# Optimization experiments

Measured on AMD Instinct MI355X. Metric: run time of the kernel, lower is better.

The kernel has to match this reference:

```python
import jax, jax.numpy as jnp
import numpy as np

B, N, D = 64, 512, 768


def setup_inputs() -> dict:
    key = jax.random.key(0)
    k = jax.random.split(key, 7)
    x = jax.random.normal(k[0], (B, N, D), dtype=jnp.float32)
    adj = jax.random.normal(k[1], (B, N, N), dtype=jnp.float32)
    # additive BERT-style mask: 0 for valid tokens, -10000 for padding
    lengths = jax.random.randint(k[2], (B,), N // 2, N + 1)
    valid = jnp.arange(N)[None, :] < lengths[:, None]          # [B, N]
    mask = jnp.where(valid, 0.0, -10000.0).astype(jnp.float32).reshape(B, 1, 1, N)
    roots_label = (jax.random.uniform(k[3], (B, N)) < 0.1).astype(jnp.float32)
    root_mask = valid.astype(jnp.int32)
    w_root = jax.random.normal(k[4], (D,), dtype=jnp.float32) / np.sqrt(D)
    b_root = jnp.zeros((), dtype=jnp.float32)
    return {"x": x, "adj": adj, "mask": mask, "roots_label": roots_label,
            "root_mask": root_mask, "w_root": w_root, "b_root": b_root}


def _matrix_tree_multi(scores, root):
    # scores: [B,N,N], root: [B,N]
    A = jnp.exp(scores)
    R = jnp.exp(root)
    L = jnp.sum(A, axis=1)                     # column sums (torch dim=1)
    LL = jnp.zeros_like(A).at[:, jnp.arange(A.shape[1]), jnp.arange(A.shape[1])].set(L + R) - A
    # equivalent to diag(L) - A + diag(R); keep diag of -A zeroed by set:
    LL = (jnp.apply_along_axis(jnp.diag, 1, np.zeros((1,))) if False else LL)  # no-op
    LL = jax.vmap(jnp.diag)(L + R) - A + jax.vmap(jnp.diag)(jnp.diagonal(A, axis1=1, axis2=2))
    # Recompute cleanly to match torch exactly: LL = diag(L) - A + diag(R)
    LL = jax.vmap(jnp.diag)(L) - A + jax.vmap(jnp.diag)(R)
    LL_inv = jnp.linalg.inv(LL)                # [B,N,N]
    LL_inv_diag = jnp.diagonal(LL_inv, axis1=1, axis2=2)   # [B,N]
    d0 = R * LL_inv_diag                       # root marginals [B,N]
    tmp1 = A * LL_inv_diag[:, None, :]         # A[i,j] * diag[j]
    tmp2 = A * jnp.swapaxes(LL_inv, 1, 2)      # A[i,j] * LL_inv[j,i]
    d = tmp1 - tmp2                            # edge marginals [B,N,N]
    return d, d0


def reference(x, adj, mask, roots_label, root_mask, w_root, b_root):
    root = jnp.einsum("bnd,d->bn", x, w_root) + b_root          # [B,N]
    m = mask[:, 0] / -10000.0                                    # [B,1,N], 0 valid / 1 pad
    root = jnp.maximum(root - m[:, 0, :] * 50.0, -40.0)
    scores = adj - m * 50.0 - jnp.swapaxes(m, 1, 2) * 50.0
    scores = jnp.maximum(scores, -40.0)
    d, d0 = _matrix_tree_multi(scores, root)
    # BCE root loss
    active = root_mask.reshape(-1) == 1
    labels = jnp.where(active, roots_label.reshape(-1), 0.0).astype(jnp.float32)
    logits = jnp.clip(d0.reshape(-1), 1e-5, 1.0 - 1e-5).astype(jnp.float32)
    bce = -(labels * jnp.log(logits) + (1.0 - labels) * jnp.log(1.0 - logits))
    loss_root = jnp.mean(bce * root_mask.reshape(-1).astype(jnp.float32))
    # attention = d^T with padded key columns zeroed
    attn = jnp.swapaxes(d, 1, 2)
    pad = jnp.broadcast_to(m.astype(bool), scores.shape)         # [B,N,N]
    attn = jnp.where(pad, 0.0, attn)
    context = jnp.matmul(attn, x)                                # [B,N,D]
    return context, d, loss_root
```

## Files before the change

kernel.cpp:

```cpp
#include <hip/hip_runtime.h>
#include <cstdint>
#include <cstddef>

#define BB 64
#define NN 512
#define DD 768
#define KB 64
#define NSTEP (NN/KB)

typedef __bf16 bf16x8 __attribute__((ext_vector_type(8)));
typedef float f32x4 __attribute__((ext_vector_type(4)));
typedef unsigned short us8 __attribute__((ext_vector_type(8)));
typedef double f64x4 __attribute__((ext_vector_type(4)));
typedef double f64x2 __attribute__((ext_vector_type(2)));

__device__ __forceinline__ float aval(float adjv, float mi, float mj) {
    return expf(fmaxf(adjv - 50.f * (mi + mj), -40.f));
}

__device__ __forceinline__ unsigned short f2bf(float v) {
    union { float f; unsigned int u; } c; c.f = v;
    return (unsigned short)((c.u + 0x7fffu + ((c.u >> 16) & 1u)) >> 16);
}
__device__ __forceinline__ float bf2f(unsigned short h) {
    union { unsigned int u; float f; } c; c.u = ((unsigned int)h) << 16;
    return c.f;
}

__device__ __forceinline__ void gl_lds16(const void* g, void* l) {
    __builtin_amdgcn_global_load_lds((const __attribute__((address_space(1))) unsigned int*)g,
                                     (__attribute__((address_space(3))) unsigned int*)l, 16, 0, 0);
}

__global__ void k_root(const float* __restrict__ x, const float* __restrict__ mask,
                       const float* __restrict__ w, const float* __restrict__ br,
                       float* __restrict__ R) {
    int wave = threadIdx.x >> 6, lane = threadIdx.x & 63;
    int row = blockIdx.x * 4 + wave;
    const float* xr = x + (size_t)row * DD;
    float s = 0.f;
#pragma unroll
    for (int k = 0; k < DD / 64; ++k) s += xr[k * 64 + lane] * w[k * 64 + lane];
    for (int off = 32; off; off >>= 1) s += __shfl_down(s, off, 64);
    if (lane == 0) {
        float m = mask[row] * -1e-4f;
        float rv = fmaxf(s + br[0] - 50.f * m, -40.f);
        R[row] = expf(rv);
    }
}

__global__ void k_colsum(const float* __restrict__ adj, const float* __restrict__ mask,
                         double* __restrict__ Lp) {
    int b = blockIdx.x, chunk = blockIdx.y;
    int j = threadIdx.x;
    float mj = mask[b * NN + j] * -1e-4f;
    const float* ab = adj + (size_t)b * NN * NN;
    double acc = 0.0;
    int i0 = chunk * 128;
    for (int i = i0; i < i0 + 128; ++i) {
        float mi = mask[b * NN + i] * -1e-4f;
        acc += (double)aval(ab[(size_t)i * NN + j], mi, mj);
    }
    Lp[((size_t)b * 4 + chunk) * NN + j] = acc;
}

template <typename T>
__global__ void k_build(const float* __restrict__ adj, const float* __restrict__ mask,
                        const float* __restrict__ R, const double* __restrict__ Lp,
                        T* __restrict__ M) {
    int b = blockIdx.x >> 9;
    int r = blockIdx.x & 511;
    int c = threadIdx.x;
    float mr = mask[b * NN + r] * -1e-4f;
    float mc = mask[b * NN + c] * -1e-4f;
    size_t idx = ((size_t)b * NN + r) * NN + c;
    float a = aval(adj[idx], mr, mc);
    T v;
    if (r == c) {
        const double* lp = Lp + (size_t)b * 4 * NN;
        double L = lp[c] + lp[NN + c] + lp[2 * NN + c] + lp[3 * NN + c];
        v = (T)(L - (double)a + (double)R[b * NN + c]);
    } else {
        v = (T)(-a);
    }
    M[idx] = v;
}

template <typename T>
__global__ void k_savecol(const T* __restrict__ M, T* __restrict__ Cb, int k0) {
    int t = threadIdx.x;
    int c = t & 63, rr = t >> 6;
    int row = blockIdx.x * 4 + rr;
    int b = row >> 9, i = row & 511;
    Cb[(size_t)row * KB + c] = M[((size_t)b * NN + i) * NN + k0 + c];
}

template <typename T>
__global__ void k_invblk(const T* __restrict__ M, T* __restrict__ Bb, int k0) {
    __shared__ double pr[KB];
    __shared__ double fv[KB];
    __shared__ double pvt;
    int b = blockIdx.x;
    int r = threadIdx.x & 63, q = threadIdx.x >> 6;
    double a[16];
    const T* Mb = M + ((size_t)b * NN + k0) * NN + k0;
#pragma unroll
    for (int c = 0; c < 16; ++c) a[c] = (double)Mb[(size_t)r * NN + q * 16 + c];
    for (int k = 0; k < KB; ++k) {
        int kq = k >> 4, kc = k & 15;
        if (r == k && q == kq) pvt = a[kc];
        __syncthreads();
        double ip = 1.0 / pvt;
        if (r == k) {
#pragma unroll
            for (int c = 0; c < 16; ++c) a[c] *= ip;
            if (q == kq) a[kc] = ip;
#pragma unroll
            for (int c = 0; c < 16; ++c) pr[q * 16 + c] = a[c];
        }
        if (r != k && q == kq) fv[r] = a[kc];
        __syncthreads();
        if (r != k) {
            double f = fv[r];
#pragma unroll
            for (int c = 0; c < 16; ++c) a[c] -= f * pr[q * 16 + c];
            if (q == kq) a[kc] = -f * ip;
        }
        __syncthreads();
    }
    T* Bo = Bb + (size_t)b * KB * KB;
#pragma unroll
    for (int c = 0; c < 16; ++c) Bo[r * KB + q * 16 + c] = (T)a[c];
}

__global__ __launch_bounds__(256) void k_piv_mfma(double* __restrict__ M,
                                                  const double* __restrict__ Bb, int step) {
    __shared__ double Ms[64][66];
    int o = blockIdx.x;
    int g = (o & 7) * 64 + (o >> 3);
    int b = g >> 3, jt = g & 7;
    int t = threadIdx.x, w = t >> 6, l = t & 63;
    double* Mb = M + (size_t)b * NN * NN;
    double* Pr = Mb + (size_t)(step * 64) * NN;
    const double* Bi = Bb + (size_t)b * KB * KB;
    if (jt == step) {
        for (int i = 0; i < 16; ++i) {
            int c = i * 256 + t;
            int row = c >> 6, col = c & 63;
            Pr[(size_t)row * NN + step * 64 + col] = Bi[row * 64 + col];
        }
        return;
    }
    const double* Mg = Pr + jt * 64;
    for (int i = 0; i < 8; ++i) {
        int c = i * 256 + t;
        int row = c >> 5, ch = c & 31;
        f64x2 v = *(const f64x2*)(Mg + (size_t)row * NN + ch * 2);
        Ms[row][ch * 2] = v[0]; Ms[row][ch * 2 + 1] = v[1];
    }
    __syncthreads();
    int lr = l & 15, lg = l >> 4;
    double a[16];
#pragma unroll
    for (int kk = 0; kk < 16; ++kk) a[kk] = Bi[(w * 16 + lr) * 64 + kk * 4 + lg];
    double* Og = Pr + (size_t)(w * 16) * NN + jt * 64;
#pragma unroll
    for (int cf = 0; cf < 4; ++cf) {
        f64x4 acc = {0., 0., 0., 0.};
#pragma unroll
        for (int kk = 0; kk < 16; ++kk)
            acc = __builtin_amdgcn_mfma_f64_16x16x4f64(a[kk], Ms[kk * 4 + lg][cf * 16 + lr], acc, 0, 0, 0);
#pragma unroll
        for (int r = 0; r < 4; ++r) Og[(size_t)(lg + 4 * r) * NN + cf * 16 + lr] = acc[r];
    }
}

__global__ __launch_bounds__(256) void k_upd2(double* __restrict__ M,
                                              const double* __restrict__ Bb, int step) {
    __shared__ double Ts[64][66];
    int o = blockIdx.x;
    int g = (o & 7) * 112 + (o >> 3);
    int b = g / 14;
    int x = g % 14;
    int it = x >> 1, half = x & 1;
    if (it >= step) ++it;
    int t = threadIdx.x, w = t >> 6, l = t & 63;
    double* Mb = M + (size_t)b * NN * NN;
    {
        const double* Cg = Mb + (size_t)(it * 64) * NN + step * 64;
        for (int i = 0; i < 8; ++i) {
            int c = i * 256 + t;
            int row = c >> 5, ch = c & 31;
            f64x2 v = *(const f64x2*)(Cg + (size_t)row * NN + ch * 2);
            Ts[row][ch * 2] = -v[0]; Ts[row][ch * 2 + 1] = -v[1];
        }
    }
    __syncthreads();
    int lr = l & 15, lg = l >> 4;
    double a[16];
#pragma unroll
    for (int kk = 0; kk < 16; ++kk) a[kk] = Ts[w * 16 + lr][kk * 4 + lg];
    __syncthreads();
    int nj = half ? 3 : 4;
    for (int jj = 0; jj < nj; ++jj) {
        int jtidx = half ? 4 + jj : jj;
        int jt = (jtidx < step) ? jtidx : jtidx + 1;
        const double* Rg = Mb + (size_t)(step * 64) * NN + jt * 64;
        for (int i = 0; i < 8; ++i) {
            int c = i * 256 + t;
            int row = c >> 5, ch = c & 31;
            f64x2 v = *(const f64x2*)(Rg + (size_t)row * NN + ch * 2);
            Ts[row][ch * 2] = v[0]; Ts[row][ch * 2 + 1] = v[1];
        }
        __syncthreads();
        double* Og = Mb + (size_t)(it * 64 + w * 16) * NN + jt * 64;
#pragma unroll
        for (int cf = 0; cf < 4; ++cf) {
            int c0 = cf * 16 + lr;
            f64x4 acc;
#pragma unroll
            for (int r = 0; r < 4; ++r) acc[r] = Og[(size_t)(lg + 4 * r) * NN + c0];
#pragma unroll
            for (int kk = 0; kk < 16; ++kk)
                acc = __builtin_amdgcn_mfma_f64_16x16x4f64(a[kk], Ts[kk * 4 + lg][c0], acc, 0, 0, 0);
#pragma unroll
            for (int r = 0; r < 4; ++r) Og[(size_t)(lg + 4 * r) * NN + c0] = acc[r];
        }
        __syncthreads();
    }
    if (half) {
        const double* Bi = Bb + (size_t)b * KB * KB;
        for (int i = 0; i < 8; ++i) {
            int c = i * 256 + t;
            int row = c >> 5, ch = c & 31;
            f64x2 v = *(const f64x2*)(Bi + row * 64 + ch * 2);
            Ts[row][ch * 2] = v[0]; Ts[row][ch * 2 + 1] = v[1];
        }
        __syncthreads();
        double* Og = Mb + (size_t)(it * 64 + w * 16) * NN + step * 64;
#pragma unroll
        for (int cf = 0; cf < 4; ++cf) {
            int c0 = cf * 16 + lr;
            f64x4 acc = {0., 0., 0., 0.};
#pragma unroll
            for (int kk = 0; kk < 16; ++kk)
                acc = __builtin_amdgcn_mfma_f64_16x16x4f64(a[kk], Ts[kk * 4 + lg][c0], acc, 0, 0, 0);
#pragma unroll
            for (int r = 0; r < 4; ++r) Og[(size_t)(lg + 4 * r) * NN + c0] = acc[r];
        }
    }
}

template <typename T>
__global__ void k_pivrows(T* __restrict__ M, const T* __restrict__ Bb, int k0) {
    __shared__ double Bi[KB][KB];
    __shared__ double Mt[KB][KB + 1];
    int b = blockIdx.x, jt = blockIdx.y * 64;
    const T* Bo = Bb + (size_t)b * KB * KB;
    T* Mb = M + ((size_t)b * NN + k0) * NN;
    int t = threadIdx.x;
    for (int e = t; e < KB * KB; e += 256) {
        int rr = e >> 6, cc = e & 63;
        Bi[rr][cc] = (double)Bo[e];
        Mt[rr][cc] = (double)Mb[(size_t)rr * NN + jt + cc];
    }
    __syncthreads();
    if (blockIdx.y == (unsigned)(k0 >> 6)) {
        for (int e = t; e < KB * KB; e += 256) {
            int rr = e >> 6, cc = e & 63;
            Mb[(size_t)rr * NN + jt + cc] = (T)Bi[rr][cc];
        }
        return;
    }
    int tx = t & 15, ty = t >> 4;
    double acc[4][4] = {};
    for (int k = 0; k < KB; ++k) {
        double av[4], bv[4];
#pragma unroll
        for (int u = 0; u < 4; ++u) { av[u] = Bi[ty * 4 + u][k]; bv[u] = Mt[k][tx * 4 + u]; }
#pragma unroll
        for (int u = 0; u < 4; ++u)
#pragma unroll
            for (int v = 0; v < 4; ++v) acc[u][v] += av[u] * bv[v];
    }
#pragma unroll
    for (int u = 0; u < 4; ++u)
#pragma unroll
        for (int v = 0; v < 4; ++v)
            Mb[(size_t)(ty * 4 + u) * NN + jt + tx * 4 + v] = (T)acc[u][v];
}

template <typename T>
__global__ void k_update(T* __restrict__ M, const T* __restrict__ Cb, int k0) {
    int step = k0 >> 6;
    int it = blockIdx.y;
    if (it == step) return;
    int b = blockIdx.x, jt = blockIdx.z;
    __shared__ double Ct[KB][KB + 1];
    __shared__ double Rt[KB][KB + 1];
    int t = threadIdx.x;
    const T* Cbb = Cb + ((size_t)b * NN + it * 64) * KB;
    const T* Rb  = M + ((size_t)b * NN + k0) * NN + jt * 64;
    for (int e = t; e < KB * KB; e += 256) {
        int rr = e >> 6, cc = e & 63;
        Ct[rr][cc] = (double)Cbb[(size_t)rr * KB + cc];
        Rt[rr][cc] = (double)Rb[(size_t)rr * NN + cc];
    }
    __syncthreads();
    int tx = t & 15, ty = t >> 4;
    double acc[4][4] = {};
    for (int k = 0; k < KB; ++k) {
        double av[4], bv[4];
#pragma unroll
        for (int u = 0; u < 4; ++u) { av[u] = Ct[ty * 4 + u][k]; bv[u] = Rt[k][tx * 4 + u]; }
#pragma unroll
        for (int u = 0; u < 4; ++u)
#pragma unroll
            for (int v = 0; v < 4; ++v) acc[u][v] += av[u] * bv[v];
    }
    T* Mo = M + ((size_t)b * NN + it * 64) * NN + jt * 64;
    bool blockcol = (jt == step);
#pragma unroll
    for (int u = 0; u < 4; ++u) {
        int row = ty * 4 + u;
#pragma unroll
        for (int v = 0; v < 4; ++v) {
            int col = tx * 4 + v;
            double val = (double)Mo[(size_t)row * NN + col] - acc[u][v];
            if (blockcol) val -= Ct[row][col];
            Mo[(size_t)row * NN + col] = (T)val;
        }
    }
}

template <typename T>
__global__ void k_dgloss(const T* __restrict__ M, const float* __restrict__ R,
                         const float* __restrict__ rlab, const int* __restrict__ rmask,
                         double* __restrict__ Dg, float* __restrict__ lossp) {
    int idx = blockIdx.x * 256 + threadIdx.x;
    int b = idx >> 9, n = idx & 511;
    double xv = (double)M[((size_t)b * NN + n) * NN + n];
    Dg[idx] = xv;
    float d0 = R[idx] * (float)xv;
    float lg = fminf(fmaxf(d0, 1e-5f), 1.f - 1e-5f);
    float rm = (float)rmask[idx];
    float lab = (rmask[idx] == 1) ? rlab[idx] : 0.f;
    float bce = -(lab * logf(lg) + (1.f - lab) * logf(1.f - lg));
    __shared__ double sm[256];
    sm[threadIdx.x] = (double)(bce * rm);
    __syncthreads();
    for (int s = 128; s; s >>= 1) {
        if (threadIdx.x < s) sm[threadIdx.x] += sm[threadIdx.x + s];
        __syncthreads();
    }
    if (threadIdx.x == 0) lossp[blockIdx.x] = (float)sm[0];
}

__global__ void k_lossfin(const float* __restrict__ lossp, float* __restrict__ outv) {
    __shared__ double sm[128];
    sm[threadIdx.x] = (double)lossp[threadIdx.x];
    __syncthreads();
    for (int s = 64; s; s >>= 1) {
        if (threadIdx.x < s) sm[threadIdx.x] += sm[threadIdx.x + s];
        __syncthreads();
    }
    if (threadIdx.x == 0) outv[0] = (float)(sm[0] / (double)(BB * NN));
}

template <typename T>
__global__ void k_d(const T* __restrict__ M, const double* __restrict__ Dg,
                    const float* __restrict__ adj, const float* __restrict__ mask,
                    float* __restrict__ dout) {
    int b = blockIdx.x, i0 = blockIdx.y * 64, j0 = blockIdx.z * 64;
    __shared__ double Xt[64][65];
    int t = threadIdx.x, ii = t & 63, jj0 = t >> 6;
    const T* Mb = M + (size_t)b * NN * NN;
    for (int jj = jj0; jj < 64; jj += 4)
        Xt[jj][ii] = (double)Mb[(size_t)(j0 + jj) * NN + i0 + ii];
    __syncthreads();
    int jc = t & 63, ir0 = t >> 6;
    float mj = mask[b * NN + j0 + jc] * -1e-4f;
    double dg = Dg[b * NN + j0 + jc];
    const float* ab = adj + (size_t)b * NN * NN;
    float* db = dout + (size_t)b * NN * NN;
    for (int ir = ir0; ir < 64; ir += 4) {
        int i = i0 + ir;
        float mi = mask[b * NN + i] * -1e-4f;
        float a = aval(ab[(size_t)i * NN + j0 + jc], mi, mj);
        db[(size_t)i * NN + j0 + jc] = a * (float)(dg - Xt[jc][ir]);
    }
}

template <typename T>
__global__ void k_d2(const T* __restrict__ M, const double* __restrict__ Dg,
                     const float* __restrict__ adj, const float* __restrict__ mask,
                     float* __restrict__ dout,
                     unsigned short* __restrict__ ATh, unsigned short* __restrict__ ATl) {
    int b = blockIdx.x, i0 = blockIdx.y * 64, j0 = blockIdx.z * 64;
    __shared__ float Xt[64][65];
    __shared__ float dt[64][65];
    int t = threadIdx.x, ii = t & 63, jj0 = t >> 6;
    const T* Mb = M + (size_t)b * NN * NN;
    for (int jj = jj0; jj < 64; jj += 4)
        Xt[jj][ii] = (float)Mb[(size_t)(j0 + jj) * NN + i0 + ii];
    __syncthreads();
    int jc = t & 63, ir0 = t >> 6;
    float mj = mask[b * NN + j0 + jc] * -1e-4f;
    double dg = Dg[b * NN + j0 + jc];
    const float* ab = adj + (size_t)b * NN * NN;
    float* db = dout + (size_t)b * NN * NN;
    for (int ir = ir0; ir < 64; ir += 4) {
        int i = i0 + ir;
        float mi = mask[b * NN + i] * -1e-4f;
        float a = aval(ab[(size_t)i * NN + j0 + jc], mi, mj);
        float v = a * (float)(dg - (double)Xt[jc][ir]);
        db[(size_t)i * NN + j0 + jc] = v;
        dt[ir][jc] = v;
    }
    __syncthreads();
    int ql = t >> 2, kq = t & 3;
    us8 vh0, vh1, vl0, vl1;
#pragma unroll
    for (int u = 0; u < 16; ++u) {
        int k = kq * 16 + u;
        float mk = mask[b * NN + i0 + k] * -1e-4f;
        float v = (mk > 0.5f) ? 0.f : dt[k][ql];
        unsigned short h = f2bf(v);
        unsigned short lo = f2bf(v - bf2f(h));
        if (u < 8) { vh0[u] = h; vl0[u] = lo; } else { vh1[u - 8] = h; vl1[u - 8] = lo; }
    }
    size_t ao = ((size_t)b * NN + j0 + ql) * NN + i0 + kq * 16;
    *(us8*)&ATh[ao] = vh0; *(us8*)&ATh[ao + 8] = vh1;
    *(us8*)&ATl[ao] = vl0; *(us8*)&ATl[ao + 8] = vl1;
}

__global__ void k_cvt_x(const float* __restrict__ x,
                        unsigned short* __restrict__ XTh, unsigned short* __restrict__ XTl) {
    int b = blockIdx.x, k0 = blockIdx.y * 64, c0 = blockIdx.z * 64;
    __shared__ float xs[64][65];
    int t = threadIdx.x;
#pragma unroll
    for (int rep = 0; rep < 16; ++rep) {
        int e = rep * 256 + t;
        int row = e >> 6, col = e & 63;
        xs[row][col] = x[((size_t)b * NN + k0 + row) * DD + c0 + col];
    }
    __syncthreads();
    int cl = t >> 2, kq = t & 3;
    us8 vh0, vh1, vl0, vl1;
#pragma unroll
    for (int u = 0; u < 16; ++u) {
        int k = kq * 16 + u;
        float v = xs[k][cl];
        unsigned short h = f2bf(v);
        unsigned short lo = f2bf(v - bf2f(h));
        if (u < 8) { vh0[u] = h; vl0[u] = lo; } else { vh1[u - 8] = h; vl1[u - 8] = lo; }
    }
    size_t ao = ((size_t)b * DD + c0 + cl) * NN + k0 + kq * 16;
    *(us8*)&XTh[ao] = vh0; *(us8*)&XTh[ao + 8] = vh1;
    *(us8*)&XTl[ao] = vl0; *(us8*)&XTl[ao + 8] = vl1;
}

__global__ __launch_bounds__(256) void k_ctx6(const unsigned short* __restrict__ ATh,
                                              const unsigned short* __restrict__ ATl,
                                              const unsigned short* __restrict__ XTh,
                                              const unsigned short* __restrict__ XTl,
                                              float* __restrict__ ctx) {
    __shared__ __align__(16) unsigned short ABs[2][128 * 64];
    __shared__ __align__(16) unsigned short Xs[2][128 * 64];
    int o = blockIdx.x;
    int g = (o & 7) * 192 + (o >> 3);
    int b = g / 24;
    int rem = g % 24;
    int bm = (rem / 6) * 128, bn = (rem % 6) * 128;
    int t = threadIdx.x, wid = t >> 6, lane = t & 63;
    f32x4 acc[4][4];
#pragma unroll
    for (int i = 0; i < 4; ++i)
#pragma unroll
        for (int j = 0; j < 4; ++j) acc[i][j] = (f32x4){0.f, 0.f, 0.f, 0.f};

    const unsigned short* Agh = ATh + ((size_t)b * NN + bm) * NN;
    const unsigned short* Agl = ATl + ((size_t)b * NN + bm) * NN;
    const unsigned short* Xgh = XTh + ((size_t)b * DD + bn) * NN;
    const unsigned short* Xgl = XTl + ((size_t)b * DD + bn) * NN;

    int m0 = (wid >> 1) * 64, n0 = (wid & 1) * 64;
    int kc = lane >> 4;

    auto STAGE = [&](int kt, int buf) {
        int ki = kt * 32;
#pragma unroll
        for (int it2 = 0; it2 < 4; ++it2) {
            int chunk = it2 * 256 + wid * 64 + lane;
            int row = chunk >> 3;
            int gs = (chunk & 7) ^ (row & 7);
            const unsigned short* s = (gs < 4) ? Agh + (size_t)row * NN + ki + gs * 8
                                               : Agl + (size_t)row * NN + ki + (gs - 4) * 8;
            gl_lds16(s, &ABs[buf][(it2 * 256 + wid * 64) * 8]);
        }
#pragma unroll
        for (int it2 = 0; it2 < 4; ++it2) {
            int chunk = it2 * 256 + wid * 64 + lane;
            int row = chunk >> 3;
            int gs = (chunk & 7) ^ (row & 7);
            const unsigned short* s = (gs < 4) ? Xgh + (size_t)row * NN + ki + gs * 8
                                               : Xgl + (size_t)row * NN + ki + (gs - 4) * 8;
            gl_lds16(s, &Xs[buf][(it2 * 256 + wid * 64) * 8]);
        }
    };

    STAGE(0, 0);
    int cur = 0;
    for (int kt = 0; kt < 16; ++kt) {
        if (kt + 1 < 16) {
            STAGE(kt + 1, cur ^ 1);
            asm volatile("s_waitcnt vmcnt(8)" ::: "memory");
        } else {
            asm volatile("s_waitcnt vmcnt(0)" ::: "memory");
        }
        __builtin_amdgcn_s_barrier();
        bf16x8 ah[4], al[4], xh[4], xl[4];
#pragma unroll
        for (int f = 0; f < 4; ++f) {
            int ar = m0 + f * 16 + (lane & 15);
            ah[f] = *(const bf16x8*)&ABs[cur][(ar * 8 + (kc ^ (ar & 7))) * 8];
            al[f] = *(const bf16x8*)&ABs[cur][(ar * 8 + ((kc | 4) ^ (ar & 7))) * 8];
            int br = n0 + f * 16 + (lane & 15);
            xh[f] = *(const bf16x8*)&Xs[cur][(br * 8 + (kc ^ (br & 7))) * 8];
            xl[f] = *(const bf16x8*)&Xs[cur][(br * 8 + ((kc | 4) ^ (br & 7))) * 8];
        }
#pragma unroll
        for (int fm = 0; fm < 4; ++fm)
#pragma unroll
            for (int fn = 0; fn < 4; ++fn)
                acc[fm][fn] = __builtin_amdgcn_mfma_f32_16x16x32_bf16(ah[fm], xh[fn], acc[fm][fn], 0, 0, 0);
#pragma unroll
        for (int fm = 0; fm < 4; ++fm)
#pragma unroll
            for (int fn = 0; fn < 4; ++fn)
                acc[fm][fn] = __builtin_amdgcn_mfma_f32_16x16x32_bf16(ah[fm], xl[fn], acc[fm][fn], 0, 0, 0);
#pragma unroll
        for (int fm = 0; fm < 4; ++fm)
#pragma unroll
            for (int fn = 0; fn < 4; ++fn)
                acc[fm][fn] = __builtin_amdgcn_mfma_f32_16x16x32_bf16(al[fm], xh[fn], acc[fm][fn], 0, 0, 0);
        __builtin_amdgcn_s_barrier();
        cur ^= 1;
    }
    float* cb = ctx + ((size_t)b * NN + bm + m0) * DD + bn + n0;
#pragma unroll
    for (int fm = 0; fm < 4; ++fm)
#pragma unroll
        for (int fn = 0; fn < 4; ++fn)
#pragma unroll
            for (int r = 0; r < 4; ++r) {
                int row = fm * 16 + (lane >> 4) * 4 + r;
                int col = fn * 16 + (lane & 15);
                cb[(size_t)row * DD + col] = acc[fm][fn][r];
            }
}

__global__ void k_ctx(const float* __restrict__ dmat, const float* __restrict__ x,
                      const float* __restrict__ mask, float* __restrict__ ctx) {
    int b = blockIdx.x, i0 = blockIdx.y * 64, c0 = blockIdx.z * 64;
    __shared__ float At[32][65];
    __shared__ float Xl[32][65];
    int t = threadIdx.x;
    int tx = t & 15, ty = t >> 4;
    float acc[4][4] = {};
    const float* db = dmat + (size_t)b * NN * NN;
    const float* xb = x + (size_t)b * NN * DD;
    int li = t & 63, lk = t >> 6;
    for (int kt = 0; kt < NN; kt += 32) {
#pragma unroll
        for (int rep = 0; rep < 8; ++rep) {
            int kk = lk + rep * 4;
            float mk = mask[b * NN + kt + kk] * -1e-4f;
            float v = db[(size_t)(kt + kk) * NN + i0 + li];
            At[kk][li] = (mk > 0.5f) ? 0.f : v;
            Xl[kk][li] = xb[(size_t)(kt + kk) * DD + c0 + li];
        }
        __syncthreads();
        for (int kk = 0; kk < 32; ++kk) {
            float av[4], bv[4];
#pragma unroll
            for (int u = 0; u < 4; ++u) { av[u] = At[kk][ty * 4 + u]; bv[u] = Xl[kk][tx * 4 + u]; }
#pragma unroll
            for (int u = 0; u < 4; ++u)
#pragma unroll
                for (int v = 0; v < 4; ++v) acc[u][v] += av[u] * bv[v];
        }
        __syncthreads();
    }
    float* cb = ctx + (size_t)b * NN * DD;
#pragma unroll
    for (int u = 0; u < 4; ++u)
#pragma unroll
        for (int v = 0; v < 4; ++v)
            cb[(size_t)(i0 + ty * 4 + u) * DD + c0 + tx * 4 + v] = acc[u][v];
}

template <typename T>
static void run_old(const float* x, const float* adj, const float* mask,
                    const float* rlab, const int* rmask, const float* w, const float* br,
                    float* ctx, float* dmat, float* lossout,
                    char* ws, hipStream_t stream) {
    size_t off = 0;
    T* M  = (T*)(ws + off); off += (size_t)BB * NN * NN * sizeof(T);
    T* Cb = (T*)(ws + off); off += (size_t)BB * NN * KB * sizeof(T);
    T* Bb = (T*)(ws + off); off += (size_t)BB * KB * KB * sizeof(T);
    double* Lp = (double*)(ws + off); off += (size_t)BB * 4 * NN * 8;
    float* Rf  = (float*)(ws + off);  off += (size_t)BB * NN * 4;
    double* Dg = (double*)(ws + off); off += (size_t)BB * NN * 8;
    float* lossp = (float*)(ws + off);

    k_root<<<BB * NN / 4, 256, 0, stream>>>(x, mask, w, br, Rf);
    k_colsum<<<dim3(BB, 4), 512, 0, stream>>>(adj, mask, Lp);
    k_build<T><<<BB * NN, 512, 0, stream>>>(adj, mask, Rf, Lp, M);
    for (int s = 0; s < NSTEP; ++s) {
        int k0 = s * KB;
        k_savecol<T><<<BB * NN / 4, 256, 0, stream>>>(M, Cb, k0);
        k_invblk<T><<<BB, 256, 0, stream>>>(M, Bb, k0);
        k_pivrows<T><<<dim3(BB, 8), 256, 0, stream>>>(M, Bb, k0);
        k_update<T><<<dim3(BB, 8, 8), 256, 0, stream>>>(M, Cb, k0);
    }
    k_dgloss<T><<<BB * NN / 256, 256, 0, stream>>>(M, Rf, rlab, rmask, Dg, lossp);
    k_lossfin<<<1, 128, 0, stream>>>(lossp, lossout);
    k_d<T><<<dim3(BB, 8, 8), 256, 0, stream>>>(M, Dg, adj, mask, dmat);
    k_ctx<<<dim3(BB, 8, 12), 256, 0, stream>>>(dmat, x, mask, ctx);
}

static void run_new(const float* x, const float* adj, const float* mask,
                    const float* rlab, const int* rmask, const float* w, const float* br,
                    float* ctx, float* dmat, float* lossout,
                    char* ws, hipStream_t stream) {
    size_t off = 0;
    double* M  = (double*)(ws + off); off += (size_t)BB * NN * NN * 8;
    double* Cb = (double*)(ws + off); off += (size_t)BB * NN * KB * 8;
    double* Bb = (double*)(ws + off); off += (size_t)BB * KB * KB * 8;
    double* Lp = (double*)(ws + off); off += (size_t)BB * 4 * NN * 8;
    float* Rf  = (float*)(ws + off);  off += (size_t)BB * NN * 4;
    double* Dg = (double*)(ws + off); off += (size_t)BB * NN * 8;
    float* lossp = (float*)(ws + off); off += 4096;
    unsigned short* ATh = (unsigned short*)(ws + off); off += (size_t)BB * NN * NN * 2;
    unsigned short* ATl = (unsigned short*)(ws + off); off += (size_t)BB * NN * NN * 2;
    unsigned short* XTh = (unsigned short*)(ws);
    unsigned short* XTl = (unsigned short*)(ws + (size_t)BB * DD * NN * 2);
    (void)Cb;

    k_root<<<BB * NN / 4, 256, 0, stream>>>(x, mask, w, br, Rf);
    k_colsum<<<dim3(BB, 4), 512, 0, stream>>>(adj, mask, Lp);
    k_build<double><<<BB * NN, 512, 0, stream>>>(adj, mask, Rf, Lp, M);
    for (int s = 0; s < NSTEP; ++s) {
        k_invblk<double><<<BB, 256, 0, stream>>>(M, Bb, s * KB);
        k_piv_mfma<<<512, 256, 0, stream>>>(M, Bb, s);
        k_upd2<<<896, 256, 0, stream>>>(M, Bb, s);
    }
    k_dgloss<double><<<BB * NN / 256, 256, 0, stream>>>(M, Rf, rlab, rmask, Dg, lossp);
    k_lossfin<<<1, 128, 0, stream>>>(lossp, lossout);
    k_d2<double><<<dim3(BB, 8, 8), 256, 0, stream>>>(M, Dg, adj, mask, dmat, ATh, ATl);
    k_cvt_x<<<dim3(BB, 8, 12), 256, 0, stream>>>(x, XTh, XTl);
    k_ctx6<<<1536, 256, 0, stream>>>(ATh, ATl, XTh, XTl, ctx);
}

extern "C" void kernel_launch(void* const* d_in, const int* in_sizes, int n_in,
                              void* d_out, int out_size, void* d_ws, size_t ws_size,
                              hipStream_t stream) {
    const float* x    = (const float*)d_in[0];
    const float* adj  = (const float*)d_in[1];
    const float* mask = (const float*)d_in[2];
    const float* rlab = (const float*)d_in[3];
    const int*   rmask= (const int*)d_in[4];
    const float* w    = (const float*)d_in[5];
    const float* br   = (const float*)d_in[6];
    float* out = (float*)d_out;
    float* ctx = out;
    float* dmat = out + (size_t)BB * NN * DD;
    float* lossout = dmat + (size_t)BB * NN * NN;
    char* ws = (char*)d_ws;

    size_t base = (size_t)BB * NN * NN * 8 + (size_t)BB * NN * KB * 8 + (size_t)BB * KB * KB * 8
                + (size_t)BB * 4 * NN * 8 + (size_t)BB * NN * 4 + (size_t)BB * NN * 8 + 4096;
    size_t need_new = base + (size_t)BB * NN * NN * 4;
    if (ws_size >= need_new)
        run_new(x, adj, mask, rlab, rmask, w, br, ctx, dmat, lossout, ws, stream);
    else if (ws_size >= base)
        run_old<double>(x, adj, mask, rlab, rmask, w, br, ctx, dmat, lossout, ws, stream);
    else
        run_old<float>(x, adj, mask, rlab, rmask, w, br, ctx, dmat, lossout, ws, stream);
}
```

Baseline: 1.178 ms.

## Switch blocked Gauss-Jordan inversion from 64-wide to 128-wide pivot blocks

The blocked in-place Gauss-Jordan inverse now uses 128-wide pivot blocks, so it runs 4 steps instead of 8. That halves the kernel launches and the passes over the 512x512 matrix per batch. A 1024-thread kernel inverts each 128x128 diagonal block. The off-diagonal column panel is saved to a scratch buffer first, so the update kernel can read the original values while the pivot row is overwritten. The update kernel also prefetches the next row tile into registers while the MFMA work on the current tile runs. In exchange, the serial 128-step diagonal inversion is longer, register pressure is higher, and the ATh workspace is reused as the scratch buffer.

```diff
diff --git a/kernel.cpp b/kernel.cpp
--- a/kernel.cpp
+++ b/kernel.cpp
@@ -133,120 +133,214 @@
     for (int c = 0; c < 16; ++c) Bo[r * KB + q * 16 + c] = (T)a[c];
 }
 
-__global__ __launch_bounds__(256) void k_piv_mfma(double* __restrict__ M,
-                                                  const double* __restrict__ Bb, int step) {
-    __shared__ double Ms[64][66];
+__global__ __launch_bounds__(1024) void k_inv128(const double* __restrict__ M,
+                                                 double* __restrict__ Dinv, int S) {
+    __shared__ double pr[128];
+    __shared__ double fv[128];
+    __shared__ double pvt;
+    int b = blockIdx.x;
+    int r = threadIdx.x & 127, q = threadIdx.x >> 7;
+    double a[16];
+    const double* Mb = M + ((size_t)b * NN + S * 128) * NN + S * 128;
+#pragma unroll
+    for (int c = 0; c < 16; ++c) a[c] = Mb[(size_t)r * NN + q * 16 + c];
+    for (int k = 0; k < 128; ++k) {
+        int kq = k >> 4, kc = k & 15;
+        if (r == k && q == kq) pvt = a[kc];
+        __syncthreads();
+        double ip = 1.0 / pvt;
+        if (r == k) {
+#pragma unroll
+            for (int c = 0; c < 16; ++c) a[c] *= ip;
+            if (q == kq) a[kc] = ip;
+#pragma unroll
+            for (int c = 0; c < 16; ++c) pr[q * 16 + c] = a[c];
+        }
+        if (r != k && q == kq) fv[r] = a[kc];
+        __syncthreads();
+        if (r != k) {
+            double f = fv[r];
+#pragma unroll
+            for (int c = 0; c < 16; ++c) a[c] -= f * pr[q * 16 + c];
+            if (q == kq) a[kc] = -f * ip;
+        }
+        __syncthreads();
+    }
+    double* Bo = Dinv + (size_t)b * 128 * 128;
+#pragma unroll
+    for (int c = 0; c < 16; ++c) Bo[r * 128 + q * 16 + c] = a[c];
+}
+
+__global__ __launch_bounds__(256) void k_savec128(const double* __restrict__ M,
+                                                  double* __restrict__ Csave, int S) {
+    int g = blockIdx.x;
+    int b = g / 6, itr = g % 6;
+    int it = (itr < 2 * S) ? itr : itr + 2;
+    int t = threadIdx.x;
+    const double* src = M + ((size_t)b * NN + it * 64) * NN + S * 128;
+    double* dst = Csave + (size_t)(b * 6 + itr) * 64 * 128;
+    for (int i = 0; i < 16; ++i) {
+        int c = i * 256 + t;
+        int row = c >> 6, ch = c & 63;
+        f64x2 v = *(const f64x2*)(src + (size_t)row * NN + ch * 2);
+        *(f64x2*)(dst + (size_t)row * 128 + ch * 2) = v;
+    }
+}
+
+__global__ __launch_bounds__(256) void k_piv128(double* __restrict__ M,
+                                                const double* __restrict__ Dinv, int S) {
+    __shared__ double Sb[2][64][66];
     int o = blockIdx.x;
     int g = (o & 7) * 64 + (o >> 3);
     int b = g >> 3, jt = g & 7;
     int t = threadIdx.x, w = t >> 6, l = t & 63;
+    int lr = l & 15, lg = l >> 4;
     double* Mb = M + (size_t)b * NN * NN;
-    double* Pr = Mb + (size_t)(step * 64) * NN;
-    const double* Bi = Bb + (size_t)b * KB * KB;
-    if (jt == step) {
+    const double* Di = Dinv + (size_t)b * 128 * 128;
+    if ((jt >> 1) == S) {
+        int hc = (jt & 1) * 64;
         for (int i = 0; i < 16; ++i) {
             int c = i * 256 + t;
-            int row = c >> 6, col = c & 63;
-            Pr[(size_t)row * NN + step * 64 + col] = Bi[row * 64 + col];
+            int row = c >> 5, ch = c & 31;
+            f64x2 v = *(const f64x2*)(Di + (size_t)row * 128 + hc + ch * 2);
+            *(f64x2*)(Mb + (size_t)(S * 128 + row) * NN + jt * 64 + ch * 2) = v;
         }
         return;
     }
-    const double* Mg = Pr + jt * 64;
-    for (int i = 0; i < 8; ++i) {
-        int c = i * 256 + t;
-        int row = c >> 5, ch = c & 31;
-        f64x2 v = *(const f64x2*)(Mg + (size_t)row * NN + ch * 2);
-        Ms[row][ch * 2] = v[0]; Ms[row][ch * 2 + 1] = v[1];
-    }
-    __syncthreads();
-    int lr = l & 15, lg = l >> 4;
-    double a[16];
-#pragma unroll
-    for (int kk = 0; kk < 16; ++kk) a[kk] = Bi[(w * 16 + lr) * 64 + kk * 4 + lg];
-    double* Og = Pr + (size_t)(w * 16) * NN + jt * 64;
-#pragma unroll
-    for (int cf = 0; cf < 4; ++cf) {
-        f64x4 acc = {0., 0., 0., 0.};
-#pragma unroll
-        for (int kk = 0; kk < 16; ++kk)
-            acc = __builtin_amdgcn_mfma_f64_16x16x4f64(a[kk], Ms[kk * 4 + lg][cf * 16 + lr], acc, 0, 0, 0);
-#pragma unroll
-        for (int r = 0; r < 4; ++r) Og[(size_t)(lg + 4 * r) * NN + cf * 16 + lr] = acc[r];
-    }
-}
-
-__global__ __launch_bounds__(256) void k_upd2(double* __restrict__ M,
-                                              const double* __restrict__ Bb, int step) {
-    __shared__ double Ts[64][66];
-    int o = blockIdx.x;
-    int g = (o & 7) * 112 + (o >> 3);
-    int b = g / 14;
-    int x = g % 14;
-    int it = x >> 1, half = x & 1;
-    if (it >= step) ++it;
-    int t = threadIdx.x, w = t >> 6, l = t & 63;
-    double* Mb = M + (size_t)b * NN * NN;
-    {
-        const double* Cg = Mb + (size_t)(it * 64) * NN + step * 64;
+    for (int h = 0; h < 2; ++h) {
+        const double* src = Mb + (size_t)(S * 128 + h * 64) * NN + jt * 64;
         for (int i = 0; i < 8; ++i) {
             int c = i * 256 + t;
             int row = c >> 5, ch = c & 31;
-            f64x2 v = *(const f64x2*)(Cg + (size_t)row * NN + ch * 2);
-            Ts[row][ch * 2] = -v[0]; Ts[row][ch * 2 + 1] = -v[1];
-        }
-    }
-    __syncthreads();
+            f64x2 v = *(const f64x2*)(src + (size_t)row * NN + ch * 2);
+            Sb[h][row][ch * 2] = v[0]; Sb[h][row][ch * 2 + 1] = v[1];
+        }
+    }
+    double aA[2][32];
+#pragma unroll
+    for (int rf = 0; rf < 2; ++rf)
+#pragma unroll
+        for (int kk = 0; kk < 32; ++kk)
+            aA[rf][kk] = Di[(size_t)(w * 32 + rf * 16 + lr) * 128 + kk * 4 + lg];
+    __syncthreads();
+#pragma unroll
+    for (int rf = 0; rf < 2; ++rf) {
+        double* Og = Mb + (size_t)(S * 128 + w * 32 + rf * 16) * NN + jt * 64;
+#pragma unroll
+        for (int cf = 0; cf < 4; ++cf) {
+            int c0 = cf * 16 + lr;
+            f64x4 acc = {0., 0., 0., 0.};
+#pragma unroll
+            for (int kk = 0; kk < 32; ++kk) {
+                int k = kk * 4 + lg;
+                double bv = Sb[k >> 6][k & 63][c0];
+                acc = __builtin_amdgcn_mfma_f64_16x16x4f64(aA[rf][kk], bv, acc, 0, 0, 0);
+            }
+#pragma unroll
+            for (int r = 0; r < 4; ++r) Og[(size_t)(lg + 4 * r) * NN + c0] = acc[r];
+        }
+    }
+}
+
+__global__ __launch_bounds__(256) void k_upd128(double* __restrict__ M,
+                                                const double* __restrict__ Dinv,
+                                                const double* __restrict__ Csave, int S) {
+    __shared__ double Sb[2][64][66];
+    int o = blockIdx.x;
+    int g = (o & 7) * 96 + (o >> 3);
+    int b = g / 12;
+    int x = g % 12;
+    int itr = x >> 1, half = x & 1;
+    int it = (itr < 2 * S) ? itr : itr + 2;
+    int t = threadIdx.x, w = t >> 6, l = t & 63;
     int lr = l & 15, lg = l >> 4;
-    double a[16];
-#pragma unroll
-    for (int kk = 0; kk < 16; ++kk) a[kk] = Ts[w * 16 + lr][kk * 4 + lg];
-    __syncthreads();
-    int nj = half ? 3 : 4;
-    for (int jj = 0; jj < nj; ++jj) {
-        int jtidx = half ? 4 + jj : jj;
-        int jt = (jtidx < step) ? jtidx : jtidx + 1;
-        const double* Rg = Mb + (size_t)(step * 64) * NN + jt * 64;
+    double* Mb = M + (size_t)b * NN * NN;
+    const double* Di = Dinv + (size_t)b * 128 * 128;
+    const double* Cg = Csave + (size_t)(b * 6 + itr) * 64 * 128;
+
+    for (int h = 0; h < 2; ++h) {
         for (int i = 0; i < 8; ++i) {
             int c = i * 256 + t;
             int row = c >> 5, ch = c & 31;
-            f64x2 v = *(const f64x2*)(Rg + (size_t)row * NN + ch * 2);
-            Ts[row][ch * 2] = v[0]; Ts[row][ch * 2 + 1] = v[1];
-        }
-        __syncthreads();
-        double* Og = Mb + (size_t)(it * 64 + w * 16) * NN + jt * 64;
-#pragma unroll
-        for (int cf = 0; cf < 4; ++cf) {
-            int c0 = cf * 16 + lr;
-            f64x4 acc;
-#pragma unroll
-            for (int r = 0; r < 4; ++r) acc[r] = Og[(size_t)(lg + 4 * r) * NN + c0];
-#pragma unroll
-            for (int kk = 0; kk < 16; ++kk)
-                acc = __builtin_amdgcn_mfma_f64_16x16x4f64(a[kk], Ts[kk * 4 + lg][c0], acc, 0, 0, 0);
-#pragma unroll
-            for (int r = 0; r < 4; ++r) Og[(size_t)(lg + 4 * r) * NN + c0] = acc[r];
-        }
-        __syncthreads();
-    }
-    if (half) {
-        const double* Bi = Bb + (size_t)b * KB * KB;
-        for (int i = 0; i < 8; ++i) {
-            int c = i * 256 + t;
-            int row = c >> 5, ch = c & 31;
-            f64x2 v = *(const f64x2*)(Bi + row * 64 + ch * 2);
-            Ts[row][ch * 2] = v[0]; Ts[row][ch * 2 + 1] = v[1];
-        }
-        __syncthreads();
-        double* Og = Mb + (size_t)(it * 64 + w * 16) * NN + step * 64;
+            f64x2 v = *(const f64x2*)(Cg + (size_t)row * 128 + h * 64 + ch * 2);
+            Sb[h][row][ch * 2] = v[0]; Sb[h][row][ch * 2 + 1] = v[1];
+        }
+    }
+    __syncthreads();
+    double aA[32];
+#pragma unroll
+    for (int kk = 0; kk < 32; ++kk) {
+        int k = kk * 4 + lg;
+        aA[kk] = -Sb[k >> 6][w * 16 + lr][k & 63];
+    }
+    __syncthreads();
+
+    auto jobsrc = [&](int j, int h, const double*& src, size_t& stride, int& jcol) {
+        if (j < 3) {
+            int jtr = half * 3 + j;
+            int jta = (jtr < 2 * S) ? jtr : jtr + 2;
+            jcol = jta * 64;
+            src = Mb + (size_t)(S * 128 + h * 64) * NN + jcol;
+            stride = NN;
+        } else {
+            jcol = (2 * S + half) * 64;
+            src = Di + (size_t)(h * 64) * 128 + half * 64;
+            stride = 128;
+        }
+    };
+
+    f64x2 rg[16];
+    auto LOADJ = [&](int j) {
+        const double* src; size_t stride; int jcol;
+        for (int h = 0; h < 2; ++h) {
+            jobsrc(j, h, src, stride, jcol);
+            for (int i = 0; i < 8; ++i) {
+                int c = i * 256 + t;
+                int row = c >> 5, ch = c & 31;
+                rg[h * 8 + i] = *(const f64x2*)(src + (size_t)row * stride + ch * 2);
+            }
+        }
+    };
+    auto WRITEJ = [&]() {
+        for (int h = 0; h < 2; ++h)
+            for (int i = 0; i < 8; ++i) {
+                int c = i * 256 + t;
+                int row = c >> 5, ch = c & 31;
+                Sb[h][row][ch * 2] = rg[h * 8 + i][0];
+                Sb[h][row][ch * 2 + 1] = rg[h * 8 + i][1];
+            }
+    };
+
+    LOADJ(0);
+    WRITEJ();
+    __syncthreads();
+    for (int j = 0; j < 4; ++j) {
+        if (j + 1 < 4) LOADJ(j + 1);
+        const double* dsrc; size_t dstride; int jcol;
+        jobsrc(j, 0, dsrc, dstride, jcol);
+        bool init = (j < 3);
+        double* Og = Mb + (size_t)(it * 64 + w * 16) * NN + jcol;
 #pragma unroll
         for (int cf = 0; cf < 4; ++cf) {
             int c0 = cf * 16 + lr;
             f64x4 acc = {0., 0., 0., 0.};
-#pragma unroll
-            for (int kk = 0; kk < 16; ++kk)
-                acc = __builtin_amdgcn_mfma_f64_16x16x4f64(a[kk], Ts[kk * 4 + lg][c0], acc, 0, 0, 0);
+            if (init) {
+#pragma unroll
+                for (int r = 0; r < 4; ++r) acc[r] = Og[(size_t)(lg + 4 * r) * NN + c0];
+            }
+#pragma unroll
+            for (int kk = 0; kk < 32; ++kk) {
+                int k = kk * 4 + lg;
+                double bv = Sb[k >> 6][k & 63][c0];
+                acc = __builtin_amdgcn_mfma_f64_16x16x4f64(aA[kk], bv, acc, 0, 0, 0);
+            }
 #pragma unroll
             for (int r = 0; r < 4; ++r) Og[(size_t)(lg + 4 * r) * NN + c0] = acc[r];
+        }
+        __syncthreads();
+        if (j + 1 < 4) {
+            WRITEJ();
+            __syncthreads();
         }
     }
 }
@@ -647,15 +741,18 @@
     unsigned short* ATl = (unsigned short*)(ws + off); off += (size_t)BB * NN * NN * 2;
     unsigned short* XTh = (unsigned short*)(ws);
     unsigned short* XTl = (unsigned short*)(ws + (size_t)BB * DD * NN * 2);
-    (void)Cb;
+    double* Dinv  = Cb;
+    double* Csave = (double*)ATh;
+    (void)Bb;
 
     k_root<<<BB * NN / 4, 256, 0, stream>>>(x, mask, w, br, Rf);
     k_colsum<<<dim3(BB, 4), 512, 0, stream>>>(adj, mask, Lp);
     k_build<double><<<BB * NN, 512, 0, stream>>>(adj, mask, Rf, Lp, M);
-    for (int s = 0; s < NSTEP; ++s) {
-        k_invblk<double><<<BB, 256, 0, stream>>>(M, Bb, s * KB);
-        k_piv_mfma<<<512, 256, 0, stream>>>(M, Bb, s);
-        k_upd2<<<896, 256, 0, stream>>>(M, Bb, s);
+    for (int S = 0; S < 4; ++S) {
+        k_savec128<<<BB * 6, 256, 0, stream>>>(M, Csave, S);
+        k_inv128<<<BB, 1024, 0, stream>>>(M, Dinv, S);
+        k_piv128<<<512, 256, 0, stream>>>(M, Dinv, S);
+        k_upd128<<<768, 256, 0, stream>>>(M, Dinv, Csave, S);
     }
     k_dgloss<double><<<BB * NN / 256, 256, 0, stream>>>(M, Rf, rlab, rmask, Dg, lossp);
     k_lossfin<<<1, 128, 0, stream>>>(lossp, lossout);
```

After: 1.565 ms. +32.8%, slower.
